# Optimization experiments

Hardware: AMD Instinct MI355X
Metric: run time of the kernel (lower is better)

The kernel has to match this reference:

```python
import jax, jax.numpy as jnp
import numpy as np

N_NODES = 50000
N_EDGES = 1600000
NEG_SLOPE = 0.2


def _gat_layer(x, src, dst, W, a_src, a_dst, b, n_nodes):
    # PyG GATConv (heads=1, concat=True): h = xW; e_ij = LeakyReLU(a_src.h_j + a_dst.h_i)
    # alpha = softmax over incoming edges of each target i; out_i = sum_j alpha_ij h_j + b
    h = x @ W                                   # [N, out]
    alpha_src = h @ a_src                        # [N]
    alpha_dst = h @ a_dst                        # [N]
    e = alpha_src[src] + alpha_dst[dst]          # [E]
    e = jnp.where(e > 0, e, NEG_SLOPE * e)       # leaky_relu(0.2)
    m = jax.ops.segment_max(e, dst, num_segments=n_nodes)   # per-target max
    ex = jnp.exp(e - m[dst])
    denom = jax.ops.segment_sum(ex, dst, num_segments=n_nodes)
    alpha = ex / (denom[dst] + 1e-16)            # [E]
    out = jax.ops.segment_sum(alpha[:, None] * h[src], dst, num_segments=n_nodes)
    return out + b


def setup_inputs() -> dict:
    key = jax.random.key(0)
    ks = jax.random.split(key, 16)
    hid, out_dim, in_dim = 128, 5, 13
    x = jax.random.normal(ks[0], (N_NODES, in_dim), dtype=jnp.float32)
    edge_index = jax.random.randint(ks[1], (2, N_EDGES), 0, N_NODES, dtype=jnp.int64)
    s = 0.1
    return {
        "x": x,
        "edge_index": edge_index,
        "W1": jax.random.normal(ks[2], (in_dim, hid), dtype=jnp.float32) * s,
        "a_src1": jax.random.normal(ks[3], (hid,), dtype=jnp.float32) * s,
        "a_dst1": jax.random.normal(ks[4], (hid,), dtype=jnp.float32) * s,
        "b1": jnp.zeros((hid,), dtype=jnp.float32),
        "W2": jax.random.normal(ks[5], (hid, hid), dtype=jnp.float32) * s,
        "a_src2": jax.random.normal(ks[6], (hid,), dtype=jnp.float32) * s,
        "a_dst2": jax.random.normal(ks[7], (hid,), dtype=jnp.float32) * s,
        "b2": jnp.zeros((hid,), dtype=jnp.float32),
        "W3": jax.random.normal(ks[8], (hid, out_dim), dtype=jnp.float32) * s,
        "a_src3": jax.random.normal(ks[9], (out_dim,), dtype=jnp.float32) * s,
        "a_dst3": jax.random.normal(ks[10], (out_dim,), dtype=jnp.float32) * s,
        "b3": jnp.zeros((out_dim,), dtype=jnp.float32),
    }


def reference(x, edge_index, W1, a_src1, a_dst1, b1, W2, a_src2, a_dst2, b2,
              W3, a_src3, a_dst3, b3):
    n = x.shape[0]
    # GATConv add_self_loops=True: append (i, i) edges
    loops = jnp.arange(n, dtype=edge_index.dtype)
    src = jnp.concatenate([edge_index[0], loops])
    dst = jnp.concatenate([edge_index[1], loops])
    h = _gat_layer(x, src, dst, W1, a_src1, a_dst1, b1, n)
    h = jax.nn.relu(h)  # dropout identity in eval mode
    h = _gat_layer(h, src, dst, W2, a_src2, a_dst2, b2, n)
    h = jax.nn.relu(h)
    h = _gat_layer(h, src, dst, W3, a_src3, a_dst3, b3, n)
    return jax.nn.log_softmax(h, axis=1)
```

## Files before the change

kernel.cpp:

```cpp
#include <hip/hip_runtime.h>
#include <hip/hip_bf16.h>


#define LEAKY(e) ((e) > 0.f ? (e) : 0.2f * (e))
__device__ inline float clamp30(float e) { return fminf(fmaxf(e, -30.f), 30.f); }
__device__ inline float expc(float e) { return __expf(clamp30(LEAKY(e))); }

__device__ inline float ldany(const void* p, int bf, int i) {
    return bf ? __bfloat162float(((const __hip_bfloat16*)p)[i])
              : ((const float*)p)[i];
}
__device__ inline int ldidx(const void* p, int i64, long long i) {
    return i64 ? (int)(((const unsigned int*)p)[2 * i])
               : ((const int*)p)[i];
}

__device__ inline float bflo(unsigned int w) { return __uint_as_float(w << 16); }
__device__ inline float bfhi(unsigned int w) { return __uint_as_float(w & 0xffff0000u); }
__device__ inline unsigned short bfbits(float a) {
    __hip_bfloat16 x = __float2bfloat16(a);
    unsigned short u; __builtin_memcpy(&u, &x, 2); return u;
}
__device__ inline unsigned int packbf(float a, float b) {
    return (unsigned int)bfbits(a) | ((unsigned int)bfbits(b) << 16);
}

__device__ inline int detect_bf(const void* W1) {
    int t = threadIdx.x & 63;
    unsigned int w = ((const unsigned int*)W1)[t];
    unsigned int e = (w >> 7) & 0xFFu;
    unsigned long long m = __ballot(e >= 0x70u && e <= 0x7Fu);
    return __popcll(m) >= 32;
}
__device__ inline int detect_i64(const void* ei) {
    int t = threadIdx.x & 63;
    unsigned int q = ((const unsigned int*)ei)[2 * t + 1];
    unsigned long long m = __ballot(q == 0u);
    return __popcll(m) >= 32;
}

typedef __attribute__((ext_vector_type(8))) short short8;
typedef __attribute__((ext_vector_type(4))) float f32x4;

__global__ __launch_bounds__(256) void fusedA(
    const void* __restrict__ xin, const void* __restrict__ ei,
    const void* __restrict__ W1, const void* __restrict__ as1,
    const void* __restrict__ ad1, const void* __restrict__ W2,
    int* __restrict__ blockHist, unsigned short* __restrict__ W2T,
    unsigned int* __restrict__ h2, float* __restrict__ asrc,
    float* __restrict__ adst, int N, int E, int NBUK)
{
    __shared__ int hist[512];
    __shared__ float Wlds[13 * 128];
    const int blk = blockIdx.x;
    const int tid = threadIdx.x;

    if (blk < 256) {
        const int i64 = detect_i64(ei);
        for (int i = tid; i < NBUK; i += 256) hist[i] = 0;
        __syncthreads();
        const int chunk = (E + 255) / 256;
        const int e0 = blk * chunk, e1 = min(e0 + chunk, E);
        for (int t = e0 + tid; t < e1; t += 256) {
            int d = ldidx(ei, i64, (long long)E + t);
            atomicAdd(&hist[d >> 7], 1);
        }
        __syncthreads();
        for (int i = tid; i < NBUK; i += 256)
            blockHist[blk * NBUK + i] = hist[i];
    } else if (blk < 1280) {
        const int bf = detect_bf(W1);
        for (int i = tid; i < 13 * 128; i += 256)
            Wlds[i] = ldany(W1, bf, i);
        __syncthreads();
        const int lane = tid & 63;
        int wave = ((blk - 256) * 256 + tid) >> 6;
        const int nw = 1024 * 4;
        float a0 = ldany(as1, bf, 2 * lane), a1 = ldany(as1, bf, 2 * lane + 1);
        float d0 = ldany(ad1, bf, 2 * lane), d1 = ldany(ad1, bf, 2 * lane + 1);
        for (int n = wave; n < N; n += nw) {
            float x0 = (lane < 13) ? ldany(xin, bf, n * 13 + lane) : 0.f;
            float s0 = 0.f, s1 = 0.f;
#pragma unroll
            for (int k = 0; k < 13; k++) {
                float xv = __shfl(x0, k);
                s0 += xv * Wlds[k * 128 + 2 * lane];
                s1 += xv * Wlds[k * 128 + 2 * lane + 1];
            }
            float pa = s0 * a0 + s1 * a1;
            float pd = s0 * d0 + s1 * d1;
#pragma unroll
            for (int o = 32; o > 0; o >>= 1) {
                pa += __shfl_xor(pa, o);
                pd += __shfl_xor(pd, o);
            }
            if (lane == 0) { asrc[n] = pa; adst[n] = pd; }
            h2[(size_t)n * 64 + lane] = packbf(s0, s1);
        }
    } else {
        const int bf = detect_bf(W1);
        for (int i = tid; i < 128 * 128; i += 256) {
            int n = i >> 7, k = i & 127;
            W2T[i] = bf ? ((const unsigned short*)W2)[k * 128 + n]
                        : bfbits(((const float*)W2)[k * 128 + n]);
        }
    }
}


__global__ __launch_bounds__(256) void sortB_prefix(
    int* __restrict__ blockHist, int* __restrict__ bucketBase, int NBUK)
{
    __shared__ int wt[4];
    __shared__ int wbase[4];
    const int b = blockIdx.x;
    const int tid = threadIdx.x, lane = tid & 63, wid = tid >> 6;
    int v = blockHist[tid * NBUK + b];
    int x = v;
#pragma unroll
    for (int o = 1; o < 64; o <<= 1) {
        int y = __shfl_up(x, o);
        if (lane >= o) x += y;
    }
    if (lane == 63) wt[wid] = x;
    __syncthreads();
    if (tid == 0) {
        int s = 0;
#pragma unroll
        for (int i = 0; i < 4; i++) { wbase[i] = s; s += wt[i]; }
        bucketBase[b] = s;
    }
    __syncthreads();
    blockHist[tid * NBUK + b] = x - v + wbase[wid];
}

__global__ __launch_bounds__(512) void sortB2_scan(
    int* __restrict__ bucketBase, int NBUK)
{
    __shared__ int wt[8];
    __shared__ int wbase[8];
    __shared__ int total_s;
    const int tid = threadIdx.x, lane = tid & 63, wid = tid >> 6;
    int v = (tid < NBUK) ? bucketBase[tid] : 0;
    int x = v;
#pragma unroll
    for (int o = 1; o < 64; o <<= 1) {
        int y = __shfl_up(x, o);
        if (lane >= o) x += y;
    }
    if (lane == 63) wt[wid] = x;
    __syncthreads();
    if (tid == 0) {
        int s = 0;
#pragma unroll
        for (int i = 0; i < 8; i++) { wbase[i] = s; s += wt[i]; }
        total_s = s;
    }
    __syncthreads();
    if (tid < NBUK) bucketBase[tid] = x - v + wbase[wid];
    if (tid == 0) bucketBase[NBUK] = total_s;
}

__global__ __launch_bounds__(256) void sortC_scatter(
    const void* __restrict__ ei,
    const int* __restrict__ blockHist, const int* __restrict__ bucketBase,
    unsigned int* __restrict__ pairbuf, int E, int NBUK)
{
    __shared__ int cur[512];
    const int i64 = detect_i64(ei);
    const int tid = threadIdx.x, blk = blockIdx.x;
    for (int i = tid; i < NBUK; i += 256)
        cur[i] = blockHist[blk * NBUK + i] + bucketBase[i];
    __syncthreads();
    const int chunk = (E + 255) / 256;
    const int e0 = blk * chunk, e1 = min(e0 + chunk, E);
    for (int t = e0 + tid; t < e1; t += 256) {
        int s = ldidx(ei, i64, t);
        int d = ldidx(ei, i64, (long long)E + t);
        int pos = atomicAdd(&cur[d >> 7], 1);
        pairbuf[pos] = ((unsigned int)(d & 127) << 16) | (unsigned int)s;
    }
}

__global__ __launch_bounds__(256) void sortD_bin(
    const unsigned int* __restrict__ pairbuf, const int* __restrict__ bucketBase,
    int* __restrict__ rowptr, unsigned short* __restrict__ ssrc, int N, int NBUK)
{
    __shared__ int cnt[128];
    __shared__ int cur2[128];
    __shared__ int wt1;
    const int b = blockIdx.x;
    const int tid = threadIdx.x, lane = tid & 63;
    const int e0 = bucketBase[b], e1 = bucketBase[b + 1];
    if (tid < 128) cnt[tid] = 0;
    __syncthreads();
    for (int i = e0 + tid; i < e1; i += 256)
        atomicAdd(&cnt[pairbuf[i] >> 16], 1);
    __syncthreads();
    if (tid < 128) {
        int v = cnt[tid];
        int x = v;
#pragma unroll
        for (int o = 1; o < 64; o <<= 1) {
            int y = __shfl_up(x, o);
            if (lane >= o) x += y;
        }
        if (tid == 63) wt1 = x;
        __syncthreads();
        if (tid >= 64) x += wt1;
        int pfx = x - v;
        cur2[tid] = pfx;
        int node = b * 128 + tid;
        if (node < N) rowptr[node] = e0 + pfx;
    } else {
        __syncthreads();
    }
    if (b == NBUK - 1 && tid == 0) rowptr[N] = e1;
    __syncthreads();
    for (int i = e0 + tid; i < e1; i += 256) {
        unsigned int w = pairbuf[i];
        int p = atomicAdd(&cur2[w >> 16], 1);
        ssrc[e0 + p] = (unsigned short)(w & 0xFFFFu);
    }
}

__global__ __launch_bounds__(256) void gemm_mfma(
    const float* __restrict__ X, const unsigned short* __restrict__ W2T,
    const void* __restrict__ asg, const void* __restrict__ adg,
    const void* __restrict__ dref, unsigned int* __restrict__ h2,
    float* __restrict__ asrc, float* __restrict__ adst, int N)
{
    const int bf = detect_bf(dref);
    __shared__ unsigned short A_s[64 * 136];
    __shared__ unsigned short B_s[128 * 136];
    const int tid = threadIdx.x;
    const int nb0 = blockIdx.x * 64;

#pragma unroll
    for (int it = 0; it < 8; it++) {
        int f = it * 256 + tid;
        int n = f >> 4, kc = (f & 15) * 8;
        uint4 v = *(const uint4*)&W2T[n * 128 + kc];
        *(uint4*)&B_s[n * 136 + kc] = v;
    }
#pragma unroll
    for (int it = 0; it < 8; it++) {
        int f = it * 256 + tid;
        int n = f >> 5, g = f & 31;
        int node = min(nb0 + n, N - 1);
        float4 v = *(const float4*)&X[(size_t)node * 128 + g * 4];
        unsigned int* dst = (unsigned int*)&A_s[n * 136 + g * 4];
        dst[0] = packbf(v.x, v.y);
        dst[1] = packbf(v.z, v.w);
    }
    __syncthreads();

    const int wv = tid >> 6;
    const int lane = tid & 63;
    const int m = lane & 15, quad = lane >> 4;

    f32x4 acc[8];
#pragma unroll
    for (int c = 0; c < 8; c++) acc[c] = (f32x4){0.f, 0.f, 0.f, 0.f};

#pragma unroll
    for (int q = 0; q < 4; q++) {
        short8 a = *(const short8*)&A_s[(wv * 16 + m) * 136 + q * 32 + quad * 8];
#pragma unroll
        for (int c = 0; c < 8; c++) {
            short8 b = *(const short8*)&B_s[(c * 16 + m) * 136 + q * 32 + quad * 8];
            acc[c] = __builtin_amdgcn_mfma_f32_16x16x32_bf16(a, b, acc[c], 0, 0, 0);
        }
    }

    float asv[8], adv[8];
#pragma unroll
    for (int c = 0; c < 8; c++) {
        asv[c] = ldany(asg, bf, c * 16 + m);
        adv[c] = ldany(adg, bf, c * 16 + m);
    }
    unsigned short* h2u = (unsigned short*)h2;
#pragma unroll
    for (int reg = 0; reg < 4; reg++) {
        int node = nb0 + wv * 16 + quad * 4 + reg;
        float pa = 0.f, pd = 0.f;
#pragma unroll
        for (int c = 0; c < 8; c++) {
            float v = acc[c][reg];
            pa += v * asv[c];
            pd += v * adv[c];
            if (node < N) h2u[(size_t)node * 128 + c * 16 + m] = bfbits(v);
        }
#pragma unroll
        for (int o = 1; o < 16; o <<= 1) {
            pa += __shfl_xor(pa, o);
            pd += __shfl_xor(pd, o);
        }
        if (node < N && m == 0) { asrc[node] = pa; adst[node] = pd; }
    }
}


__device__ inline int rdl(int v, int j) { return __builtin_amdgcn_readlane(v, j); }
__device__ inline float rdlf(float v, int j) {
    return __uint_as_float((unsigned int)__builtin_amdgcn_readlane((int)__float_as_uint(v), j));
}

__device__ inline float2 agg_node(
    int n, const int* rowptr, const unsigned short* ssrc,
    const unsigned int* h2, const float* asrc, const float* adst,
    float bx, float by, unsigned ul)
{
    const int lane = (int)ul;
    float ad = adst[n];
    float wself = expc(asrc[n] + ad);
    unsigned int hw = h2[((unsigned)n << 6) | ul];
    float accx = wself * bflo(hw), accy = wself * bfhi(hw);
    float wpart = (lane == 0) ? wself : 0.f;
    const int start = rowptr[n], end = rowptr[n + 1];
    for (int base = start; base < end; base += 64) {
        int sl = 0;
        float wl = 0.f;
        if (base + lane < end) {
            sl = (int)ssrc[base + lane];
            wl = expc(asrc[sl] + ad);
        }
        wpart += wl;
        const int cnt = min(64, end - base);
        int j = 0;
        for (; j + 16 <= cnt; j += 16) {
            unsigned int u[16];
            float w[16];
#pragma unroll
            for (int t = 0; t < 16; t++) {
                unsigned s = (unsigned)rdl(sl, j + t);
                u[t] = h2[(s << 6) | ul];
            }
#pragma unroll
            for (int t = 0; t < 16; t++) w[t] = rdlf(wl, j + t);
#pragma unroll
            for (int t = 0; t < 16; t++) {
                accx += w[t] * bflo(u[t]);
                accy += w[t] * bfhi(u[t]);
            }
        }
        for (; j + 8 <= cnt; j += 8) {
            unsigned int u[8];
            float w[8];
#pragma unroll
            for (int t = 0; t < 8; t++) {
                unsigned s = (unsigned)rdl(sl, j + t);
                u[t] = h2[(s << 6) | ul];
            }
#pragma unroll
            for (int t = 0; t < 8; t++) w[t] = rdlf(wl, j + t);
#pragma unroll
            for (int t = 0; t < 8; t++) {
                accx += w[t] * bflo(u[t]);
                accy += w[t] * bfhi(u[t]);
            }
        }
        for (; j < cnt; j++) {
            unsigned s = (unsigned)rdl(sl, j);
            float w = rdlf(wl, j);
            unsigned int ww = h2[(s << 6) | ul];
            accx += w * bflo(ww);
            accy += w * bfhi(ww);
        }
    }
    float wsum = wpart;
#pragma unroll
    for (int o = 32; o > 0; o >>= 1) wsum += __shfl_xor(wsum, o);
    float inv = 1.f / (wsum + 1e-16f);
    float2 ov = {fmaxf(accx * inv + bx, 0.f), fmaxf(accy * inv + by, 0.f)};
    return ov;
}

__global__ __launch_bounds__(256) void agg_fused128(
    const int* __restrict__ rowptr, const unsigned short* __restrict__ ssrc,
    const unsigned int* __restrict__ h2, const float* __restrict__ asrc,
    const float* __restrict__ adst, const void* __restrict__ bias,
    const void* __restrict__ dref, float* __restrict__ feat, int N)
{
    const int bf = detect_bf(dref);
    const int lane = threadIdx.x & 63;
    int wave = (blockIdx.x * 256 + threadIdx.x) >> 6;
    int nw = (gridDim.x * 256) >> 6;
    const float bx = ldany(bias, bf, 2 * lane);
    const float by = ldany(bias, bf, 2 * lane + 1);
    const unsigned ul = (unsigned)lane;
    for (int n = wave; n < N; n += nw) {
        float2 ov = agg_node(n, rowptr, ssrc, h2, asrc, adst, bx, by, ul);
        *(float2*)&feat[(size_t)n * 128 + 2 * lane] = ov;
    }
}

__global__ __launch_bounds__(256) void agg_fused128_proj(
    const int* __restrict__ rowptr, const unsigned short* __restrict__ ssrc,
    const unsigned int* __restrict__ h2, const float* __restrict__ asrc,
    const float* __restrict__ adst, const void* __restrict__ bias,
    const void* __restrict__ dref,
    const void* __restrict__ W3, const void* __restrict__ as3,
    const void* __restrict__ ad3,
    float* __restrict__ h3p, float* __restrict__ asrc3, float* __restrict__ adst3,
    int N)
{
    const int bf = detect_bf(dref);
    __shared__ float WpT[7 * 128];
    const int tid = threadIdx.x;
    for (int i = tid; i < 7 * 128; i += 256) {
        int j = i >> 7, k = i & 127;
        float v;
        if (j < 5) v = ldany(W3, bf, k * 5 + j);
        else if (j == 5) v = ldany(as3, bf, k);
        else v = ldany(ad3, bf, k);
        WpT[i] = v;
    }
    __syncthreads();
    const int lane = tid & 63;
    int wave = (blockIdx.x * 256 + tid) >> 6;
    int nw = (gridDim.x * 256) >> 6;
    const float bx = ldany(bias, bf, 2 * lane);
    const float by = ldany(bias, bf, 2 * lane + 1);
    const unsigned ul = (unsigned)lane;
    for (int n = wave; n < N; n += nw) {
        float2 ov = agg_node(n, rowptr, ssrc, h2, asrc, adst, bx, by, ul);
        float p[7];
#pragma unroll
        for (int j = 0; j < 7; j++)
            p[j] = ov.x * WpT[j * 128 + 2 * lane] + ov.y * WpT[j * 128 + 2 * lane + 1];
#pragma unroll
        for (int o = 32; o > 0; o >>= 1) {
#pragma unroll
            for (int j = 0; j < 7; j++) p[j] += __shfl_xor(p[j], o);
        }
        if (lane == 0) {
            float4 o0 = {p[0], p[1], p[2], p[3]};
            *(float4*)&h3p[(size_t)n * 8] = o0;
            h3p[(size_t)n * 8 + 4] = p[4];
            asrc3[n] = p[5];
            adst3[n] = p[6];
        }
    }
}

__global__ __launch_bounds__(256) void agg_fused5(
    const int* __restrict__ rowptr, const unsigned short* __restrict__ ssrc,
    const float* __restrict__ h3p, const float* __restrict__ asrc,
    const float* __restrict__ adst, const void* __restrict__ b3,
    const void* __restrict__ dref, float* __restrict__ out, int N)
{
    const int bf = detect_bf(dref);
    const int lane = threadIdx.x & 63;
    int wave = (blockIdx.x * 256 + threadIdx.x) >> 6;
    int nw = (gridDim.x * 256) >> 6;

    for (int n = wave; n < N; n += nw) {
        float ad = adst[n];
        float a0 = 0.f, a1 = 0.f, a2 = 0.f, a3 = 0.f, a4 = 0.f, wsum = 0.f;
        if (lane == 0) {
            float w = expc(asrc[n] + ad);
            wsum = w;
            float4 v = *(const float4*)&h3p[(unsigned)n * 8u];
            float v4 = h3p[(unsigned)n * 8u + 4u];
            a0 = w * v.x; a1 = w * v.y; a2 = w * v.z; a3 = w * v.w; a4 = w * v4;
        }
        const int start = rowptr[n], end = rowptr[n + 1];
        for (int i = start + lane; i < end; i += 64) {
            unsigned s = (unsigned)ssrc[i];
            float w = expc(asrc[s] + ad);
            float4 v = *(const float4*)&h3p[s * 8u];
            float v4 = h3p[s * 8u + 4u];
            wsum += w;
            a0 += w * v.x; a1 += w * v.y; a2 += w * v.z; a3 += w * v.w; a4 += w * v4;
        }
#pragma unroll
        for (int o = 32; o > 0; o >>= 1) {
            a0 += __shfl_xor(a0, o); a1 += __shfl_xor(a1, o); a2 += __shfl_xor(a2, o);
            a3 += __shfl_xor(a3, o); a4 += __shfl_xor(a4, o); wsum += __shfl_xor(wsum, o);
        }
        if (lane == 0) {
            float inv = 1.f / (wsum + 1e-16f);
            float v0 = a0 * inv + ldany(b3, bf, 0);
            float v1 = a1 * inv + ldany(b3, bf, 1);
            float v2 = a2 * inv + ldany(b3, bf, 2);
            float v3 = a3 * inv + ldany(b3, bf, 3);
            float v4 = a4 * inv + ldany(b3, bf, 4);
            float m = fmaxf(fmaxf(fmaxf(v0, v1), fmaxf(v2, v3)), v4);
            float s = __expf(v0 - m) + __expf(v1 - m) + __expf(v2 - m)
                    + __expf(v3 - m) + __expf(v4 - m);
            float lse = m + __logf(s);
            out[n * 5 + 0] = v0 - lse; out[n * 5 + 1] = v1 - lse;
            out[n * 5 + 2] = v2 - lse; out[n * 5 + 3] = v3 - lse;
            out[n * 5 + 4] = v4 - lse;
        }
    }
}

extern "C" void kernel_launch(void* const* d_in, const int* in_sizes, int n_in,
                              void* d_out, int out_size, void* d_ws, size_t ws_size,
                              hipStream_t stream)
{
    const void* x  = d_in[0];
    const void* ei = d_in[1];
    const void* W1 = d_in[2];
    const void* as1= d_in[3];
    const void* ad1= d_in[4];
    const void* b1 = d_in[5];
    const void* W2 = d_in[6];
    const void* as2= d_in[7];
    const void* ad2= d_in[8];
    const void* b2 = d_in[9];
    const void* W3 = d_in[10];
    const void* as3= d_in[11];
    const void* ad3= d_in[12];
    const void* b3 = d_in[13];

    const int N = in_sizes[0] / 13;
    const int E = in_sizes[1] / 2;
    const int NBUK = (N + 127) / 128;

    float* ws    = (float*)d_ws;
    float* feat  = ws;
    unsigned int* h2 = (unsigned int*)(feat + (size_t)N * 128);
    float* asrc  = (float*)(h2 + (size_t)N * 64);
    float* adst  = asrc + N;
    float* asrc3 = adst + N;
    float* adst3 = asrc3 + N;
    float* h3p   = adst3 + N;
    int*   rowptr= (int*)(h3p + (size_t)N * 8);
    int*   bucketBase = rowptr + N + 1;
    int*   blockHist  = bucketBase + NBUK + 1;
    unsigned short* W2T = (unsigned short*)(blockHist + 256 * NBUK);
    unsigned int* pairbuf = (unsigned int*)(W2T + 128 * 128);
    unsigned short* ssrc16 = (unsigned short*)(pairbuf + E);

    const int wb = (N + 3) / 4;
    const int gb = (N + 63) / 64;

    fusedA<<<1281, 256, 0, stream>>>(x, ei, W1, as1, ad1, W2,
                                     blockHist, W2T, h2, asrc, adst, N, E, NBUK);
    sortB_prefix<<<NBUK, 256, 0, stream>>>(blockHist, bucketBase, NBUK);
    sortB2_scan<<<1, 512, 0, stream>>>(bucketBase, NBUK);
    sortC_scatter<<<256, 256, 0, stream>>>(ei, blockHist, bucketBase, pairbuf, E, NBUK);
    sortD_bin<<<NBUK, 256, 0, stream>>>(pairbuf, bucketBase, rowptr, ssrc16, N, NBUK);

    agg_fused128<<<wb, 256, 0, stream>>>(rowptr, ssrc16, h2, asrc, adst, b1, W1,
                                         feat, N);
    gemm_mfma<<<gb, 256, 0, stream>>>(feat, W2T, as2, ad2, W1, h2, asrc, adst, N);
    agg_fused128_proj<<<wb, 256, 0, stream>>>(rowptr, ssrc16, h2, asrc, adst, b2, W1,
                                              W3, as3, ad3, h3p, asrc3, adst3, N);
    agg_fused5<<<wb, 256, 0, stream>>>(rowptr, ssrc16, h3p, asrc3, adst3, b3, W1,
                                       (float*)d_out, N);
}
```

Measured before the change: 286.8 us.

## Merge sort scan kernels, store layer-1 features as bf16, pack asrc3 into h3p

Merges the two prefix-scan kernels into one, using a last-block-done atomic counter so the final block runs the global bucket scan. Layer-1 aggregation output is stored as packed bf16 instead of fp32, which halves that write and the GEMM's read and removes conversion work in the GEMM load. The layer-3 projection stores asrc3 in the spare slot of the 8-float h3p row, so the last aggregation gets it in the same gathered load, and a new lane-parallel reduction lets several lanes write the results. The cost is an extra counter reset and threadfences, plus a small precision change because the bf16 rounding now happens at a different point.

```diff
diff --git a/kernel.cpp b/kernel.cpp
--- a/kernel.cpp
+++ b/kernel.cpp
@@ -48,7 +48,7 @@
     const void* __restrict__ ad1, const void* __restrict__ W2,
     int* __restrict__ blockHist, unsigned short* __restrict__ W2T,
     unsigned int* __restrict__ h2, float* __restrict__ asrc,
-    float* __restrict__ adst, int N, int E, int NBUK)
+    float* __restrict__ adst, int* __restrict__ counter, int N, int E, int NBUK)
 {
     __shared__ int hist[512];
     __shared__ float Wlds[13 * 128];
@@ -99,6 +99,7 @@
         }
     } else {
         const int bf = detect_bf(W1);
+        if (tid == 0) *counter = 0;
         for (int i = tid; i < 128 * 128; i += 256) {
             int n = i >> 7, k = i & 127;
             W2T[i] = bf ? ((const unsigned short*)W2)[k * 128 + n]
@@ -107,15 +108,18 @@
     }
 }
 
-
-__global__ __launch_bounds__(256) void sortB_prefix(
-    int* __restrict__ blockHist, int* __restrict__ bucketBase, int NBUK)
-{
-    __shared__ int wt[4];
-    __shared__ int wbase[4];
+__global__ __launch_bounds__(512) void sortB_all(
+    int* __restrict__ blockHist, int* __restrict__ bucketBase,
+    int* __restrict__ counter, int NBUK)
+{
+    __shared__ int wt[8];
+    __shared__ int wbase[8];
+    __shared__ int total_s;
+    __shared__ int isLast;
     const int b = blockIdx.x;
     const int tid = threadIdx.x, lane = tid & 63, wid = tid >> 6;
-    int v = blockHist[tid * NBUK + b];
+
+    int v = (tid < 256) ? blockHist[tid * NBUK + b] : 0;
     int x = v;
 #pragma unroll
     for (int o = 1; o < 64; o <<= 1) {
@@ -127,28 +131,30 @@
     if (tid == 0) {
         int s = 0;
 #pragma unroll
-        for (int i = 0; i < 4; i++) { wbase[i] = s; s += wt[i]; }
-        bucketBase[b] = s;
-    }
-    __syncthreads();
-    blockHist[tid * NBUK + b] = x - v + wbase[wid];
-}
-
-__global__ __launch_bounds__(512) void sortB2_scan(
-    int* __restrict__ bucketBase, int NBUK)
-{
-    __shared__ int wt[8];
-    __shared__ int wbase[8];
-    __shared__ int total_s;
-    const int tid = threadIdx.x, lane = tid & 63, wid = tid >> 6;
-    int v = (tid < NBUK) ? bucketBase[tid] : 0;
-    int x = v;
+        for (int i = 0; i < 8; i++) { wbase[i] = s; s += wt[i]; }
+        total_s = s;
+    }
+    __syncthreads();
+    if (tid < 256) blockHist[tid * NBUK + b] = x - v + wbase[wid];
+    if (tid == 0) bucketBase[b] = total_s;
+
+    __threadfence();
+    if (tid == 0) {
+        int prev = atomicAdd(counter, 1);
+        isLast = (prev == NBUK - 1);
+    }
+    __syncthreads();
+    if (!isLast) return;
+    __threadfence();
+
+    int v2 = (tid < NBUK) ? atomicAdd(&bucketBase[tid], 0) : 0;
+    int x2 = v2;
 #pragma unroll
     for (int o = 1; o < 64; o <<= 1) {
-        int y = __shfl_up(x, o);
-        if (lane >= o) x += y;
-    }
-    if (lane == 63) wt[wid] = x;
+        int y = __shfl_up(x2, o);
+        if (lane >= o) x2 += y;
+    }
+    if (lane == 63) wt[wid] = x2;
     __syncthreads();
     if (tid == 0) {
         int s = 0;
@@ -157,7 +163,7 @@
         total_s = s;
     }
     __syncthreads();
-    if (tid < NBUK) bucketBase[tid] = x - v + wbase[wid];
+    if (tid < NBUK) bucketBase[tid] = x2 - v2 + wbase[wid];
     if (tid == 0) bucketBase[NBUK] = total_s;
 }
 
@@ -225,7 +231,8 @@
 }
 
 __global__ __launch_bounds__(256) void gemm_mfma(
-    const float* __restrict__ X, const unsigned short* __restrict__ W2T,
+    const unsigned int* __restrict__ Xp,
+    const unsigned short* __restrict__ W2T,
     const void* __restrict__ asg, const void* __restrict__ adg,
     const void* __restrict__ dref, unsigned int* __restrict__ h2,
     float* __restrict__ asrc, float* __restrict__ adst, int N)
@@ -244,14 +251,12 @@
         *(uint4*)&B_s[n * 136 + kc] = v;
     }
 #pragma unroll
-    for (int it = 0; it < 8; it++) {
+    for (int it = 0; it < 4; it++) {
         int f = it * 256 + tid;
-        int n = f >> 5, g = f & 31;
+        int n = f >> 4, q = f & 15;
         int node = min(nb0 + n, N - 1);
-        float4 v = *(const float4*)&X[(size_t)node * 128 + g * 4];
-        unsigned int* dst = (unsigned int*)&A_s[n * 136 + g * 4];
-        dst[0] = packbf(v.x, v.y);
-        dst[1] = packbf(v.z, v.w);
+        uint4 v = *(const uint4*)&Xp[(size_t)node * 64 + q * 4];
+        *(uint4*)&A_s[n * 136 + q * 8] = v;
     }
     __syncthreads();
 
@@ -380,7 +385,7 @@
     const int* __restrict__ rowptr, const unsigned short* __restrict__ ssrc,
     const unsigned int* __restrict__ h2, const float* __restrict__ asrc,
     const float* __restrict__ adst, const void* __restrict__ bias,
-    const void* __restrict__ dref, float* __restrict__ feat, int N)
+    const void* __restrict__ dref, unsigned int* __restrict__ featp, int N)
 {
     const int bf = detect_bf(dref);
     const int lane = threadIdx.x & 63;
@@ -391,7 +396,7 @@
     const unsigned ul = (unsigned)lane;
     for (int n = wave; n < N; n += nw) {
         float2 ov = agg_node(n, rowptr, ssrc, h2, asrc, adst, bx, by, ul);
-        *(float2*)&feat[(size_t)n * 128 + 2 * lane] = ov;
+        featp[((unsigned)n << 6) | ul] = packbf(ov.x, ov.y);
     }
 }
 
@@ -402,8 +407,7 @@
     const void* __restrict__ dref,
     const void* __restrict__ W3, const void* __restrict__ as3,
     const void* __restrict__ ad3,
-    float* __restrict__ h3p, float* __restrict__ asrc3, float* __restrict__ adst3,
-    int N)
+    float* __restrict__ h3p, float* __restrict__ adst3, int N)
 {
     const int bf = detect_bf(dref);
     __shared__ float WpT[7 * 128];
@@ -423,6 +427,7 @@
     const float bx = ldany(bias, bf, 2 * lane);
     const float by = ldany(bias, bf, 2 * lane + 1);
     const unsigned ul = (unsigned)lane;
+    const int g = lane & 7;
     for (int n = wave; n < N; n += nw) {
         float2 ov = agg_node(n, rowptr, ssrc, h2, asrc, adst, bx, by, ul);
         float p[7];
@@ -430,25 +435,29 @@
         for (int j = 0; j < 7; j++)
             p[j] = ov.x * WpT[j * 128 + 2 * lane] + ov.y * WpT[j * 128 + 2 * lane + 1];
 #pragma unroll
-        for (int o = 32; o > 0; o >>= 1) {
+        for (int o = 1; o < 8; o <<= 1) {
 #pragma unroll
             for (int j = 0; j < 7; j++) p[j] += __shfl_xor(p[j], o);
         }
-        if (lane == 0) {
-            float4 o0 = {p[0], p[1], p[2], p[3]};
-            *(float4*)&h3p[(size_t)n * 8] = o0;
-            h3p[(size_t)n * 8 + 4] = p[4];
-            asrc3[n] = p[5];
-            adst3[n] = p[6];
-        }
+        float v = p[0];
+        v = (g == 1) ? p[1] : v;
+        v = (g == 2) ? p[2] : v;
+        v = (g == 3) ? p[3] : v;
+        v = (g == 4) ? p[4] : v;
+        v = (g == 5) ? p[5] : v;
+        v = (g == 6) ? p[6] : v;
+#pragma unroll
+        for (int o = 8; o < 64; o <<= 1) v += __shfl_xor(v, o);
+        if (lane < 6) h3p[(size_t)n * 8 + lane] = v;
+        else if (lane == 6) adst3[n] = v;
     }
 }
 
 __global__ __launch_bounds__(256) void agg_fused5(
     const int* __restrict__ rowptr, const unsigned short* __restrict__ ssrc,
-    const float* __restrict__ h3p, const float* __restrict__ asrc,
-    const float* __restrict__ adst, const void* __restrict__ b3,
-    const void* __restrict__ dref, float* __restrict__ out, int N)
+    const float* __restrict__ h3p, const float* __restrict__ adst3,
+    const void* __restrict__ b3, const void* __restrict__ dref,
+    float* __restrict__ out, int N)
 {
     const int bf = detect_bf(dref);
     const int lane = threadIdx.x & 63;
@@ -456,23 +465,23 @@
     int nw = (gridDim.x * 256) >> 6;
 
     for (int n = wave; n < N; n += nw) {
-        float ad = adst[n];
+        float ad = adst3[n];
         float a0 = 0.f, a1 = 0.f, a2 = 0.f, a3 = 0.f, a4 = 0.f, wsum = 0.f;
         if (lane == 0) {
-            float w = expc(asrc[n] + ad);
+            float4 v = *(const float4*)&h3p[(size_t)n * 8];
+            float2 v45 = *(const float2*)&h3p[(size_t)n * 8 + 4];
+            float w = expc(v45.y + ad);
             wsum = w;
-            float4 v = *(const float4*)&h3p[(unsigned)n * 8u];
-            float v4 = h3p[(unsigned)n * 8u + 4u];
-            a0 = w * v.x; a1 = w * v.y; a2 = w * v.z; a3 = w * v.w; a4 = w * v4;
+            a0 = w * v.x; a1 = w * v.y; a2 = w * v.z; a3 = w * v.w; a4 = w * v45.x;
         }
         const int start = rowptr[n], end = rowptr[n + 1];
         for (int i = start + lane; i < end; i += 64) {
             unsigned s = (unsigned)ssrc[i];
-            float w = expc(asrc[s] + ad);
-            float4 v = *(const float4*)&h3p[s * 8u];
-            float v4 = h3p[s * 8u + 4u];
+            float4 v = *(const float4*)&h3p[(size_t)s * 8];
+            float2 v45 = *(const float2*)&h3p[(size_t)s * 8 + 4];
+            float w = expc(v45.y + ad);
             wsum += w;
-            a0 += w * v.x; a1 += w * v.y; a2 += w * v.z; a3 += w * v.w; a4 += w * v4;
+            a0 += w * v.x; a1 += w * v.y; a2 += w * v.z; a3 += w * v.w; a4 += w * v45.x;
         }
 #pragma unroll
         for (int o = 32; o > 0; o >>= 1) {
@@ -521,35 +530,35 @@
     const int NBUK = (N + 127) / 128;
 
     float* ws    = (float*)d_ws;
-    float* feat  = ws;
-    unsigned int* h2 = (unsigned int*)(feat + (size_t)N * 128);
+    unsigned int* featp = (unsigned int*)ws;
+    unsigned int* h2 = featp + (size_t)N * 64;
     float* asrc  = (float*)(h2 + (size_t)N * 64);
     float* adst  = asrc + N;
-    float* asrc3 = adst + N;
-    float* adst3 = asrc3 + N;
+    float* adst3 = adst + N;
     float* h3p   = adst3 + N;
     int*   rowptr= (int*)(h3p + (size_t)N * 8);
     int*   bucketBase = rowptr + N + 1;
     int*   blockHist  = bucketBase + NBUK + 1;
     unsigned short* W2T = (unsigned short*)(blockHist + 256 * NBUK);
-    unsigned int* pairbuf = (unsigned int*)(W2T + 128 * 128);
+    int*   counter = (int*)(W2T + 128 * 128);
+    unsigned int* pairbuf = (unsigned int*)(counter + 1);
     unsigned short* ssrc16 = (unsigned short*)(pairbuf + E);
 
     const int wb = (N + 3) / 4;
     const int gb = (N + 63) / 64;
 
     fusedA<<<1281, 256, 0, stream>>>(x, ei, W1, as1, ad1, W2,
-                                     blockHist, W2T, h2, asrc, adst, N, E, NBUK);
-    sortB_prefix<<<NBUK, 256, 0, stream>>>(blockHist, bucketBase, NBUK);
-    sortB2_scan<<<1, 512, 0, stream>>>(bucketBase, NBUK);
+                                     blockHist, W2T, h2, asrc, adst, counter,
+                                     N, E, NBUK);
+    sortB_all<<<NBUK, 512, 0, stream>>>(blockHist, bucketBase, counter, NBUK);
     sortC_scatter<<<256, 256, 0, stream>>>(ei, blockHist, bucketBase, pairbuf, E, NBUK);
     sortD_bin<<<NBUK, 256, 0, stream>>>(pairbuf, bucketBase, rowptr, ssrc16, N, NBUK);
 
     agg_fused128<<<wb, 256, 0, stream>>>(rowptr, ssrc16, h2, asrc, adst, b1, W1,
-                                         feat, N);
-    gemm_mfma<<<gb, 256, 0, stream>>>(feat, W2T, as2, ad2, W1, h2, asrc, adst, N);
+                                         featp, N);
+    gemm_mfma<<<gb, 256, 0, stream>>>(featp, W2T, as2, ad2, W1, h2, asrc, adst, N);
     agg_fused128_proj<<<wb, 256, 0, stream>>>(rowptr, ssrc16, h2, asrc, adst, b2, W1,
-                                              W3, as3, ad3, h3p, asrc3, adst3, N);
-    agg_fused5<<<wb, 256, 0, stream>>>(rowptr, ssrc16, h3p, asrc3, adst3, b3, W1,
+                                              W3, as3, ad3, h3p, adst3, N);
+    agg_fused5<<<wb, 256, 0, stream>>>(rowptr, ssrc16, h3p, adst3, b3, W1,
                                        (float*)d_out, N);
 }
```

Result: slower. 366.0 us (+27.6%).
